# Performance work log

Measured on AMD Instinct MI355X. Metric: run time of the kernel, lower is better.

## Reference

```python
import jax, jax.numpy as jnp
import numpy as np
from jax import lax

B, T, E, H, N_LAYERS = 64, 256, 512, 512, 2


def _lstm_stack(x, params):
    # x: [B, T, in] -> returns full top-layer hidden sequence [T, B, H]
    xs = jnp.swapaxes(x, 0, 1)  # time-major [T, B, in]
    for (Wih, Whh, bih, bhh) in params:
        def step(carry, xt, Wih=Wih, Whh=Whh, bih=bih, bhh=bhh):
            h, c = carry
            gates = xt @ Wih.T + bih + h @ Whh.T + bhh  # [B, 4H]
            i, f, g, o = jnp.split(gates, 4, axis=-1)   # PyTorch gate order i,f,g,o
            i = jax.nn.sigmoid(i)
            f = jax.nn.sigmoid(f)
            g = jnp.tanh(g)
            o = jax.nn.sigmoid(o)
            c = f * c + i * g
            h = o * jnp.tanh(c)
            return (h, c), h
        nb = xs.shape[1]
        hdim = Whh.shape[1]
        init = (jnp.zeros((nb, hdim), xs.dtype), jnp.zeros((nb, hdim), xs.dtype))
        _, xs = lax.scan(step, init, xs)
    return xs  # [T, B, H]


def setup_inputs() -> dict:
    key = jax.random.key(0)
    ks = jax.random.split(key, 16)
    s = 0.04  # ~1/sqrt(H) init scale
    inp = {"text": jax.random.normal(ks[0], (B, T, E), dtype=jnp.float32)}
    # layer 0: input dim E; layer 1: input dim H
    inp["W_ih0"] = jax.random.normal(ks[1], (4 * H, E), dtype=jnp.float32) * s
    inp["W_hh0"] = jax.random.normal(ks[2], (4 * H, H), dtype=jnp.float32) * s
    inp["b_ih0"] = jax.random.normal(ks[3], (4 * H,), dtype=jnp.float32) * s
    inp["b_hh0"] = jax.random.normal(ks[4], (4 * H,), dtype=jnp.float32) * s
    inp["W_ih1"] = jax.random.normal(ks[5], (4 * H, H), dtype=jnp.float32) * s
    inp["W_hh1"] = jax.random.normal(ks[6], (4 * H, H), dtype=jnp.float32) * s
    inp["b_ih1"] = jax.random.normal(ks[7], (4 * H,), dtype=jnp.float32) * s
    inp["b_hh1"] = jax.random.normal(ks[8], (4 * H,), dtype=jnp.float32) * s
    inp["W_lin"] = jax.random.normal(ks[9], (1, 2 * H), dtype=jnp.float32) * s
    inp["b_lin"] = jax.random.normal(ks[10], (1,), dtype=jnp.float32) * s
    return inp


def reference(text, W_ih0, W_hh0, b_ih0, b_hh0, W_ih1, W_hh1, b_ih1, b_hh1, W_lin, b_lin):
    params = [(W_ih0, W_hh0, b_ih0, b_hh0), (W_ih1, W_hh1, b_ih1, b_hh1)]
    out_f = _lstm_stack(text, params)[-1]                       # [B, H] last step, fwd pass
    out_r = _lstm_stack(jnp.flip(text, axis=1), params)[-1]     # [B, H] last step, reversed input (same weights, as in source)
    out = jnp.concatenate([out_f, out_r], axis=1)               # [B, 2H]
    # dropout is identity in eval mode
    return out @ W_lin.T + b_lin                                # [B, 1]
```

## Files before the change

kernel.cpp:

```cpp
#include <hip/hip_runtime.h>
#include <stdint.h>

constexpr int HD   = 512;
constexpr int TS   = 256;
constexpr int NB   = 64;
constexpr int MBR  = 128;
constexpr int SLAB = MBR * HD;

typedef __attribute__((ext_vector_type(8))) short bf16x8;
typedef __attribute__((ext_vector_type(4))) float f32x4;

__device__ __forceinline__ unsigned short f2bf(float f){
  union { float f; unsigned u; } v; v.f = f;
  unsigned r = v.u + 0x7fffu + ((v.u >> 16) & 1u);
  return (unsigned short)(r >> 16);
}
__device__ __forceinline__ float fsig(float x){ return 1.f / (1.f + __expf(-x)); }
__device__ __forceinline__ float ftanh(float x){ return 1.f - 2.f / (__expf(2.f * x) + 1.f); }
__device__ __forceinline__ void vdrain(){ asm volatile("s_waitcnt vmcnt(0)" ::: "memory"); }

__device__ __forceinline__ int ld_flag_sc1(const int* p){
  int v;
  asm volatile("global_load_dword %0, %1, off sc0 sc1\n\ts_waitcnt vmcnt(0)"
               : "=v"(v) : "v"(p) : "memory");
  return v;
}
__device__ __forceinline__ void st_sc1_b32(void* p, int v){
  asm volatile("global_store_dword %0, %1, off sc0 sc1" :: "v"(p), "v"(v) : "memory");
}

#define LD16_DEF(NAME, TAIL)                                                    \
__device__ __forceinline__ void NAME(const void* p, f32x4* r){                  \
  asm volatile(                                                                 \
    "global_load_dwordx4 %0,  %16, off sc0 sc1\n\t"                             \
    "global_load_dwordx4 %1,  %16, off offset:64 sc0 sc1\n\t"                   \
    "global_load_dwordx4 %2,  %16, off offset:128 sc0 sc1\n\t"                  \
    "global_load_dwordx4 %3,  %16, off offset:192 sc0 sc1\n\t"                  \
    "global_load_dwordx4 %4,  %16, off offset:256 sc0 sc1\n\t"                  \
    "global_load_dwordx4 %5,  %16, off offset:320 sc0 sc1\n\t"                  \
    "global_load_dwordx4 %6,  %16, off offset:384 sc0 sc1\n\t"                  \
    "global_load_dwordx4 %7,  %16, off offset:448 sc0 sc1\n\t"                  \
    "global_load_dwordx4 %8,  %16, off offset:512 sc0 sc1\n\t"                  \
    "global_load_dwordx4 %9,  %16, off offset:576 sc0 sc1\n\t"                  \
    "global_load_dwordx4 %10, %16, off offset:640 sc0 sc1\n\t"                  \
    "global_load_dwordx4 %11, %16, off offset:704 sc0 sc1\n\t"                  \
    "global_load_dwordx4 %12, %16, off offset:768 sc0 sc1\n\t"                  \
    "global_load_dwordx4 %13, %16, off offset:832 sc0 sc1\n\t"                  \
    "global_load_dwordx4 %14, %16, off offset:896 sc0 sc1\n\t"                  \
    "global_load_dwordx4 %15, %16, off offset:960 sc0 sc1\n\t"                  \
    TAIL                                                                        \
    : "=&v"(r[0]), "=&v"(r[1]), "=&v"(r[2]), "=&v"(r[3]),                       \
      "=&v"(r[4]), "=&v"(r[5]), "=&v"(r[6]), "=&v"(r[7]),                       \
      "=&v"(r[8]), "=&v"(r[9]), "=&v"(r[10]), "=&v"(r[11]),                     \
      "=&v"(r[12]), "=&v"(r[13]), "=&v"(r[14]), "=&v"(r[15])                    \
    : "v"(p) : "memory");                                                       \
}
LD16_DEF(ld16_sc1,       "s_waitcnt vmcnt(0)")
LD16_DEF(ld16_sc1_issue, "s_nop 0")

__device__ __forceinline__ bf16x8 pack8(float4 a, float4 b){
  bf16x8 w;
  w[0]=(short)f2bf(a.x); w[1]=(short)f2bf(a.y); w[2]=(short)f2bf(a.z); w[3]=(short)f2bf(a.w);
  w[4]=(short)f2bf(b.x); w[5]=(short)f2bf(b.y); w[6]=(short)f2bf(b.z); w[7]=(short)f2bf(b.w);
  return w;
}

__global__ __launch_bounds__(512, 1)
void lstm_persist(const float* __restrict__ text,
                  const float* __restrict__ Wih0, const float* __restrict__ Whh0,
                  const float* __restrict__ bih0, const float* __restrict__ bhh0,
                  const float* __restrict__ Wih1, const float* __restrict__ Whh1,
                  const float* __restrict__ bih1, const float* __restrict__ bhh1,
                  unsigned short* __restrict__ h0x,
                  unsigned short* __restrict__ h1r,
                  float* __restrict__ H1f,
                  int* __restrict__ F)
{
  extern __shared__ unsigned short Blds[];
  __shared__ int s_abort;

  const int wg    = blockIdx.x;
  const int layer = wg >> 7;
  const int grp   = (wg >> 5) & 3;
  const int slice = wg & 31;
  const int m0    = grp * 32;
  const int u0    = slice * 16;
  const int tid   = threadIdx.x;
  const int wv    = tid >> 6;
  const int l     = tid & 63;
  const int lj    = l & 15;
  const int lk    = l >> 4;
  const int wgrp  = wv & 3;
  const int mi    = wv >> 2;

  if (tid == 0) s_abort = 0;

  int* F0g = F + (0 + grp) * (TS * 32);
  int* F1g = F + (4 + grp) * (TS * 32);

  const float* Wihl = layer ? Wih1 : Wih0;
  const float* Whhl = layer ? Whh1 : Whh0;
  for (int it = tid; it < 64 * 128; it += 512){
    int c = it >> 7, kg = it & 127;
    int unit = u0 + ((c >> 4) << 2) + ((c & 15) >> 2);
    int gate = c & 3;
    const float* s = (kg < 64) ? (Wihl + (size_t)(gate * HD + unit) * HD + kg * 8)
                               : (Whhl + (size_t)(gate * HD + unit) * HD + (kg - 64) * 8);
    *(bf16x8*)((char*)Blds + c * 2048 + ((kg ^ (c & 7)) << 4)) =
        pack8(((const float4*)s)[0], ((const float4*)s)[1]);
  }

  const int myunit = u0 + (wgrp << 2) + (lj >> 2);
  const int mygate = lj & 3;
  const float bgv  = (layer ? bih1 : bih0)[mygate * HD + myunit]
                   + (layer ? bhh1 : bhh0)[mygate * HD + myunit];
  const int aoff   = (m0 + mi * 16 + lj) * HD + lk * 8;
  const int cboff  = (wgrp * 16 + lj) * 2048;
  const int swz    = lj & 7;

  float cst[4] = {0.f, 0.f, 0.f, 0.f};
  __syncthreads();

  auto ldsB = [&](int kg)->bf16x8 {
    return *(const bf16x8*)((const char*)Blds + cboff + ((kg ^ swz) << 4));
  };
  auto pollwait = [&](const int* pA, const int* pB){
    if (*(volatile int*)&s_abort) return;
    const int* fp = (l < 32) ? (pA + l) : (pB + (l - 32));
    int it = 0;
    for (;;){
      int v = ld_flag_sc1(fp);
      if (__all(v != 0)) break;
      if (++it > 2000000){ s_abort = 1; break; }
      __builtin_amdgcn_s_sleep(1);
    }
  };
  auto cellstore = [&](const f32x4& aP, const f32x4& aQ,
                       unsigned short* __restrict__ hslab, bool wrF){
    #pragma unroll
    for (int r = 0; r < 4; ++r){
      float v  = aP[r] + aQ[r] + bgv;
      float v1 = __shfl_xor(v, 1);
      float v2 = __shfl_xor(v, 2);
      float v3 = __shfl_xor(v, 3);
      auto pick = [&](int m)->float {
        return m == 0 ? v : (m == 1 ? v1 : (m == 2 ? v2 : v3));
      };
      float gi = pick(mygate);
      float gf = pick(mygate ^ 1);
      float gg = pick(mygate ^ 2);
      float go = pick(mygate ^ 3);
      float i_ = fsig(gi);
      float f_ = fsig(gf);
      float g_ = ftanh(gg);
      float o_ = fsig(go);
      float c  = f_ * cst[r] + i_ * g_;
      cst[r] = c;
      float h  = o_ * ftanh(c);
      int row  = m0 + mi * 16 + lk * 4 + r;
      int hb   = (int)f2bf(h);
      int pb   = __shfl_xor(hb, 4);
      if ((lj & 7) == 0)
        st_sc1_b32((char*)hslab + ((size_t)row * HD + myunit) * 2,
                   (hb & 0xffff) | (pb << 16));
      if (wrF && mygate == 0)
        H1f[(size_t)row * HD + myunit] = h;
    }
  };
  auto preX = [&](int t, f32x4& acc){
    int ar  = m0 + mi * 16 + lj;
    int b   = ar & 63;
    int ts2 = (ar < 64) ? t : (TS - 1 - t);
    const float* src = text + ((size_t)b * TS + ts2) * HD + lk * 8;
    acc = (f32x4){0.f, 0.f, 0.f, 0.f};
    #pragma unroll
    for (int kk = 0; kk < 16; ++kk){
      const float* s = src + kk * 32;
      bf16x8 a = pack8(((const float4*)s)[0], ((const float4*)s)[1]);
      acc = __builtin_amdgcn_mfma_f32_16x16x32_bf16(a, ldsB(kk * 4 + lk), acc, 0, 0, 0);
    }
  };

  if (layer == 0){
    f32x4 accPre;
    preX(0, accPre);
    for (int t = 0; t < TS; ++t){
      if (t > 0){
        if (wv == 0) pollwait(F0g + (t - 1) * 32, F0g + (t - 1) * 32);
        __syncthreads();
      }
      f32x4 accPost = {0.f, 0.f, 0.f, 0.f};
      if (t > 0){
        f32x4 raw[16];
        ld16_sc1(h0x + (size_t)(t - 1) * SLAB + aoff, raw);
        #pragma unroll
        for (int kk = 0; kk < 16; ++kk)
          accPost = __builtin_amdgcn_mfma_f32_16x16x32_bf16(
                      __builtin_bit_cast(bf16x8, raw[kk]), ldsB(64 + kk * 4 + lk),
                      accPost, 0, 0, 0);
      }
      cellstore(accPre, accPost, h0x + (size_t)t * SLAB, false);
      vdrain();
      __syncthreads();
      if (tid == 0) st_sc1_b32(F0g + t * 32 + slice, 1);
      if (t + 1 < TS) preX(t + 1, accPre);
    }
  } else {
    for (int t = 0; t < TS; ++t){
      if (wv == 0){
        const int* pA = (t > 0) ? (F1g + (t - 1) * 32) : (F0g + 0);
        pollwait(pA, F0g + t * 32);
      }
      __syncthreads();
      f32x4 rawI[16], rawR[16];
      if (t > 0){
        ld16_sc1_issue(h0x + (size_t)t * SLAB + aoff, rawI);
        ld16_sc1(h1r + (size_t)((t - 1) & 3) * SLAB + aoff, rawR);
      } else {
        ld16_sc1(h0x + aoff, rawI);
      }
      f32x4 accPre  = {0.f, 0.f, 0.f, 0.f};
      f32x4 accPost = {0.f, 0.f, 0.f, 0.f};
      #pragma unroll
      for (int kk = 0; kk < 16; ++kk)
        accPre = __builtin_amdgcn_mfma_f32_16x16x32_bf16(
                   __builtin_bit_cast(bf16x8, rawI[kk]), ldsB(kk * 4 + lk),
                   accPre, 0, 0, 0);
      if (t > 0){
        #pragma unroll
        for (int kk = 0; kk < 16; ++kk)
          accPost = __builtin_amdgcn_mfma_f32_16x16x32_bf16(
                      __builtin_bit_cast(bf16x8, rawR[kk]), ldsB(64 + kk * 4 + lk),
                      accPost, 0, 0, 0);
      }
      cellstore(accPre, accPost, h1r + (size_t)(t & 3) * SLAB, t == TS - 1);
      vdrain();
      __syncthreads();
      if (tid == 0) st_sc1_b32(F1g + t * 32 + slice, 1);
    }
  }
}

__global__ void final_linear(const float* __restrict__ H1f, const float* __restrict__ Wlin,
                             const float* __restrict__ blin, float* __restrict__ out){
  int b = blockIdx.x, l = threadIdx.x;
  float s = 0.f;
  for (int j = l; j < HD; j += 64) s += H1f[(size_t)b * HD + j]        * Wlin[j];
  for (int j = l; j < HD; j += 64) s += H1f[(size_t)(NB + b) * HD + j] * Wlin[HD + j];
  #pragma unroll
  for (int off = 32; off; off >>= 1) s += __shfl_down(s, off);
  if (l == 0) out[b] = s + blin[0];
}

extern "C" void kernel_launch(void* const* d_in, const int* in_sizes, int n_in,
                              void* d_out, int out_size, void* d_ws, size_t ws_size,
                              hipStream_t stream)
{
  const float* text = (const float*)d_in[0];
  const float* Wih0 = (const float*)d_in[1];
  const float* Whh0 = (const float*)d_in[2];
  const float* bih0 = (const float*)d_in[3];
  const float* bhh0 = (const float*)d_in[4];
  const float* Wih1 = (const float*)d_in[5];
  const float* Whh1 = (const float*)d_in[6];
  const float* bih1 = (const float*)d_in[7];
  const float* bhh1 = (const float*)d_in[8];
  const float* Wlin = (const float*)d_in[9];
  const float* blin = (const float*)d_in[10];

  uint8_t* p = (uint8_t*)d_ws;
  unsigned short* h0x = (unsigned short*)p; p += (size_t)TS * SLAB * 2;
  unsigned short* h1r = (unsigned short*)p; p += (size_t)4 * SLAB * 2;
  float* H1f          = (float*)p;          p += (size_t)SLAB * 4;
  int* F              = (int*)p;            p += (size_t)8 * TS * 32 * 4;

  hipMemsetAsync(F, 0, (size_t)8 * TS * 32 * 4, stream);

  hipFuncSetAttribute((const void*)lstm_persist,
                      hipFuncAttributeMaxDynamicSharedMemorySize, 131072);

  const float* A0 = text;
  const float *A1 = Wih0, *A2 = Whh0, *A3 = bih0, *A4 = bhh0;
  const float *A5 = Wih1, *A6 = Whh1, *A7 = bih1, *A8 = bhh1;
  unsigned short* B0 = h0x; unsigned short* B1 = h1r;
  float* B2 = H1f; int* B3 = F;
  void* args[] = {(void*)&A0,
                  (void*)&A1, (void*)&A2, (void*)&A3, (void*)&A4,
                  (void*)&A5, (void*)&A6, (void*)&A7, (void*)&A8,
                  (void*)&B0, (void*)&B1, (void*)&B2, (void*)&B3};
  hipLaunchCooperativeKernel((void*)lstm_persist, dim3(256), dim3(512),
                             args, 131072, stream);

  final_linear<<<NB, 64, 0, stream>>>(H1f, Wlin, blin, (float*)d_out);
}
```

Before: 3.722 ms.

## Collapse batch-row groups into each workgroup, cutting grid from 256 to 64

```diff
diff --git a/kernel.cpp b/kernel.cpp
--- a/kernel.cpp
+++ b/kernel.cpp
@@ -29,35 +29,31 @@
   asm volatile("global_store_dword %0, %1, off sc0 sc1" :: "v"(p), "v"(v) : "memory");
 }
 
-#define LD16_DEF(NAME, TAIL)                                                    \
-__device__ __forceinline__ void NAME(const void* p, f32x4* r){                  \
-  asm volatile(                                                                 \
-    "global_load_dwordx4 %0,  %16, off sc0 sc1\n\t"                             \
-    "global_load_dwordx4 %1,  %16, off offset:64 sc0 sc1\n\t"                   \
-    "global_load_dwordx4 %2,  %16, off offset:128 sc0 sc1\n\t"                  \
-    "global_load_dwordx4 %3,  %16, off offset:192 sc0 sc1\n\t"                  \
-    "global_load_dwordx4 %4,  %16, off offset:256 sc0 sc1\n\t"                  \
-    "global_load_dwordx4 %5,  %16, off offset:320 sc0 sc1\n\t"                  \
-    "global_load_dwordx4 %6,  %16, off offset:384 sc0 sc1\n\t"                  \
-    "global_load_dwordx4 %7,  %16, off offset:448 sc0 sc1\n\t"                  \
-    "global_load_dwordx4 %8,  %16, off offset:512 sc0 sc1\n\t"                  \
-    "global_load_dwordx4 %9,  %16, off offset:576 sc0 sc1\n\t"                  \
-    "global_load_dwordx4 %10, %16, off offset:640 sc0 sc1\n\t"                  \
-    "global_load_dwordx4 %11, %16, off offset:704 sc0 sc1\n\t"                  \
-    "global_load_dwordx4 %12, %16, off offset:768 sc0 sc1\n\t"                  \
-    "global_load_dwordx4 %13, %16, off offset:832 sc0 sc1\n\t"                  \
-    "global_load_dwordx4 %14, %16, off offset:896 sc0 sc1\n\t"                  \
-    "global_load_dwordx4 %15, %16, off offset:960 sc0 sc1\n\t"                  \
-    TAIL                                                                        \
-    : "=&v"(r[0]), "=&v"(r[1]), "=&v"(r[2]), "=&v"(r[3]),                       \
-      "=&v"(r[4]), "=&v"(r[5]), "=&v"(r[6]), "=&v"(r[7]),                       \
-      "=&v"(r[8]), "=&v"(r[9]), "=&v"(r[10]), "=&v"(r[11]),                     \
-      "=&v"(r[12]), "=&v"(r[13]), "=&v"(r[14]), "=&v"(r[15])                    \
-    : "v"(p) : "memory");                                                       \
-}
-LD16_DEF(ld16_sc1,       "s_waitcnt vmcnt(0)")
-LD16_DEF(ld16_sc1_issue, "s_nop 0")
-
+__device__ __forceinline__ void ld16_sc1(const void* p, f32x4* r){
+  asm volatile(
+    "global_load_dwordx4 %0,  %16, off sc0 sc1\n\t"
+    "global_load_dwordx4 %1,  %16, off offset:64 sc0 sc1\n\t"
+    "global_load_dwordx4 %2,  %16, off offset:128 sc0 sc1\n\t"
+    "global_load_dwordx4 %3,  %16, off offset:192 sc0 sc1\n\t"
+    "global_load_dwordx4 %4,  %16, off offset:256 sc0 sc1\n\t"
+    "global_load_dwordx4 %5,  %16, off offset:320 sc0 sc1\n\t"
+    "global_load_dwordx4 %6,  %16, off offset:384 sc0 sc1\n\t"
+    "global_load_dwordx4 %7,  %16, off offset:448 sc0 sc1\n\t"
+    "global_load_dwordx4 %8,  %16, off offset:512 sc0 sc1\n\t"
+    "global_load_dwordx4 %9,  %16, off offset:576 sc0 sc1\n\t"
+    "global_load_dwordx4 %10, %16, off offset:640 sc0 sc1\n\t"
+    "global_load_dwordx4 %11, %16, off offset:704 sc0 sc1\n\t"
+    "global_load_dwordx4 %12, %16, off offset:768 sc0 sc1\n\t"
+    "global_load_dwordx4 %13, %16, off offset:832 sc0 sc1\n\t"
+    "global_load_dwordx4 %14, %16, off offset:896 sc0 sc1\n\t"
+    "global_load_dwordx4 %15, %16, off offset:960 sc0 sc1\n\t"
+    "s_waitcnt vmcnt(0)"
+    : "=&v"(r[0]), "=&v"(r[1]), "=&v"(r[2]), "=&v"(r[3]),
+      "=&v"(r[4]), "=&v"(r[5]), "=&v"(r[6]), "=&v"(r[7]),
+      "=&v"(r[8]), "=&v"(r[9]), "=&v"(r[10]), "=&v"(r[11]),
+      "=&v"(r[12]), "=&v"(r[13]), "=&v"(r[14]), "=&v"(r[15])
+    : "v"(p) : "memory");
+}
 __device__ __forceinline__ bf16x8 pack8(float4 a, float4 b){
   bf16x8 w;
   w[0]=(short)f2bf(a.x); w[1]=(short)f2bf(a.y); w[2]=(short)f2bf(a.z); w[3]=(short)f2bf(a.w);
@@ -80,23 +76,20 @@
   __shared__ int s_abort;
 
   const int wg    = blockIdx.x;
-  const int layer = wg >> 7;
-  const int grp   = (wg >> 5) & 3;
+  const int layer = wg >> 5;
   const int slice = wg & 31;
-  const int m0    = grp * 32;
   const int u0    = slice * 16;
   const int tid   = threadIdx.x;
   const int wv    = tid >> 6;
   const int l     = tid & 63;
   const int lj    = l & 15;
   const int lk    = l >> 4;
-  const int wgrp  = wv & 3;
-  const int mi    = wv >> 2;
+  const int mi    = wv;
 
   if (tid == 0) s_abort = 0;
 
-  int* F0g = F + (0 + grp) * (TS * 32);
-  int* F1g = F + (4 + grp) * (TS * 32);
+  int* F0 = F;
+  int* F1 = F + TS * 32;
 
   const float* Wihl = layer ? Wih1 : Wih0;
   const float* Whhl = layer ? Whh1 : Whh0;
@@ -110,23 +103,28 @@
         pack8(((const float4*)s)[0], ((const float4*)s)[1]);
   }
 
-  const int myunit = u0 + (wgrp << 2) + (lj >> 2);
   const int mygate = lj & 3;
-  const float bgv  = (layer ? bih1 : bih0)[mygate * HD + myunit]
-                   + (layer ? bhh1 : bhh0)[mygate * HD + myunit];
-  const int aoff   = (m0 + mi * 16 + lj) * HD + lk * 8;
-  const int cboff  = (wgrp * 16 + lj) * 2048;
-  const int swz    = lj & 7;
-
-  float cst[4] = {0.f, 0.f, 0.f, 0.f};
+  const int usub   = lj >> 2;
+  float bgv[4];
+  #pragma unroll
+  for (int cf = 0; cf < 4; ++cf){
+    int unit = u0 + cf * 4 + usub;
+    bgv[cf] = (layer ? bih1 : bih0)[mygate * HD + unit]
+            + (layer ? bhh1 : bhh0)[mygate * HD + unit];
+  }
+  const int arow = mi * 16 + lj;
+  const int aoff = arow * HD + lk * 8;
+  const int swz  = lj & 7;
+
+  float cst[4][4] = {};
   __syncthreads();
 
-  auto ldsB = [&](int kg)->bf16x8 {
-    return *(const bf16x8*)((const char*)Blds + cboff + ((kg ^ swz) << 4));
-  };
-  auto pollwait = [&](const int* pA, const int* pB){
+  auto ldsB = [&](int cf, int kg)->bf16x8 {
+    return *(const bf16x8*)((const char*)Blds + (cf * 16 + lj) * 2048 + ((kg ^ swz) << 4));
+  };
+  auto pollwait = [&](const int* base){
     if (*(volatile int*)&s_abort) return;
-    const int* fp = (l < 32) ? (pA + l) : (pB + (l - 32));
+    const int* fp = base + (l & 31);
     int it = 0;
     for (;;){
       int v = ld_flag_sc1(fp);
@@ -135,108 +133,122 @@
       __builtin_amdgcn_s_sleep(1);
     }
   };
-  auto cellstore = [&](const f32x4& aP, const f32x4& aQ,
+  auto mfmaHalf = [&](const f32x4* raw, int gb, f32x4* acc){
+    #pragma unroll
+    for (int kk = 0; kk < 16; ++kk){
+      bf16x8 a = __builtin_bit_cast(bf16x8, raw[kk]);
+      #pragma unroll
+      for (int cf = 0; cf < 4; ++cf)
+        acc[cf] = __builtin_amdgcn_mfma_f32_16x16x32_bf16(
+                    a, ldsB(cf, gb + kk * 4 + lk), acc[cf], 0, 0, 0);
+    }
+  };
+  auto cellstore = [&](const f32x4* aP, const f32x4* aQ,
                        unsigned short* __restrict__ hslab, bool wrF){
     #pragma unroll
-    for (int r = 0; r < 4; ++r){
-      float v  = aP[r] + aQ[r] + bgv;
-      float v1 = __shfl_xor(v, 1);
-      float v2 = __shfl_xor(v, 2);
-      float v3 = __shfl_xor(v, 3);
-      auto pick = [&](int m)->float {
-        return m == 0 ? v : (m == 1 ? v1 : (m == 2 ? v2 : v3));
-      };
-      float gi = pick(mygate);
-      float gf = pick(mygate ^ 1);
-      float gg = pick(mygate ^ 2);
-      float go = pick(mygate ^ 3);
-      float i_ = fsig(gi);
-      float f_ = fsig(gf);
-      float g_ = ftanh(gg);
-      float o_ = fsig(go);
-      float c  = f_ * cst[r] + i_ * g_;
-      cst[r] = c;
-      float h  = o_ * ftanh(c);
-      int row  = m0 + mi * 16 + lk * 4 + r;
-      int hb   = (int)f2bf(h);
-      int pb   = __shfl_xor(hb, 4);
-      if ((lj & 7) == 0)
-        st_sc1_b32((char*)hslab + ((size_t)row * HD + myunit) * 2,
-                   (hb & 0xffff) | (pb << 16));
-      if (wrF && mygate == 0)
-        H1f[(size_t)row * HD + myunit] = h;
-    }
-  };
-  auto preX = [&](int t, f32x4& acc){
-    int ar  = m0 + mi * 16 + lj;
-    int b   = ar & 63;
-    int ts2 = (ar < 64) ? t : (TS - 1 - t);
+    for (int cf = 0; cf < 4; ++cf){
+      #pragma unroll
+      for (int r = 0; r < 4; ++r){
+        float v  = aP[cf][r] + aQ[cf][r] + bgv[cf];
+        float v1 = __shfl_xor(v, 1);
+        float v2 = __shfl_xor(v, 2);
+        float v3 = __shfl_xor(v, 3);
+        auto pick = [&](int m)->float {
+          return m == 0 ? v : (m == 1 ? v1 : (m == 2 ? v2 : v3));
+        };
+        float gi = pick(mygate);
+        float gf = pick(mygate ^ 1);
+        float gg = pick(mygate ^ 2);
+        float go = pick(mygate ^ 3);
+        float i_ = fsig(gi);
+        float f_ = fsig(gf);
+        float g_ = ftanh(gg);
+        float o_ = fsig(go);
+        float c  = f_ * cst[cf][r] + i_ * g_;
+        cst[cf][r] = c;
+        float h  = o_ * ftanh(c);
+        int row  = mi * 16 + lk * 4 + r;
+        int unit = u0 + cf * 4 + usub;
+        int hb   = (int)f2bf(h);
+        int pb   = __shfl_xor(hb, 4);
+        if ((lj & 7) == 0)
+          st_sc1_b32((char*)hslab + ((size_t)row * HD + unit) * 2,
+                     (hb & 0xffff) | (pb << 16));
+        if (wrF && mygate == 0)
+          H1f[(size_t)row * HD + unit] = h;
+      }
+    }
+  };
+  auto preX = [&](int t, f32x4* acc){
+    int b   = arow & 63;
+    int ts2 = (arow < 64) ? t : (TS - 1 - t);
     const float* src = text + ((size_t)b * TS + ts2) * HD + lk * 8;
-    acc = (f32x4){0.f, 0.f, 0.f, 0.f};
+    #pragma unroll
+    for (int cf = 0; cf < 4; ++cf) acc[cf] = (f32x4){0.f, 0.f, 0.f, 0.f};
     #pragma unroll
     for (int kk = 0; kk < 16; ++kk){
       const float* s = src + kk * 32;
       bf16x8 a = pack8(((const float4*)s)[0], ((const float4*)s)[1]);
-      acc = __builtin_amdgcn_mfma_f32_16x16x32_bf16(a, ldsB(kk * 4 + lk), acc, 0, 0, 0);
-    }
-  };
+      #pragma unroll
+      for (int cf = 0; cf < 4; ++cf)
+        acc[cf] = __builtin_amdgcn_mfma_f32_16x16x32_bf16(
+                    a, ldsB(cf, kk * 4 + lk), acc[cf], 0, 0, 0);
+    }
+  };
+
+  f32x4 accPre[4], accPost[4];
 
   if (layer == 0){
-    f32x4 accPre;
     preX(0, accPre);
     for (int t = 0; t < TS; ++t){
+      #pragma unroll
+      for (int cf = 0; cf < 4; ++cf) accPost[cf] = (f32x4){0.f, 0.f, 0.f, 0.f};
       if (t > 0){
-        if (wv == 0) pollwait(F0g + (t - 1) * 32, F0g + (t - 1) * 32);
+        if (wv == 0) pollwait(F0 + (t - 1) * 32);
         __syncthreads();
-      }
-      f32x4 accPost = {0.f, 0.f, 0.f, 0.f};
-      if (t > 0){
         f32x4 raw[16];
         ld16_sc1(h0x + (size_t)(t - 1) * SLAB + aoff, raw);
-        #pragma unroll
-        for (int kk = 0; kk < 16; ++kk)
-          accPost = __builtin_amdgcn_mfma_f32_16x16x32_bf16(
-                      __builtin_bit_cast(bf16x8, raw[kk]), ldsB(64 + kk * 4 + lk),
-                      accPost, 0, 0, 0);
+        mfmaHalf(raw, 64, accPost);
       }
       cellstore(accPre, accPost, h0x + (size_t)t * SLAB, false);
       vdrain();
       __syncthreads();
-      if (tid == 0) st_sc1_b32(F0g + t * 32 + slice, 1);
+      if (tid == 0) st_sc1_b32(F0 + t * 32 + slice, 1);
       if (t + 1 < TS) preX(t + 1, accPre);
     }
   } else {
+    if (wv == 0) pollwait(F0 + 0);
+    __syncthreads();
+    {
+      f32x4 raw[16];
+      ld16_sc1(h0x + aoff, raw);
+      #pragma unroll
+      for (int cf = 0; cf < 4; ++cf) accPre[cf] = (f32x4){0.f, 0.f, 0.f, 0.f};
+      mfmaHalf(raw, 0, accPre);
+    }
     for (int t = 0; t < TS; ++t){
-      if (wv == 0){
-        const int* pA = (t > 0) ? (F1g + (t - 1) * 32) : (F0g + 0);
-        pollwait(pA, F0g + t * 32);
-      }
-      __syncthreads();
-      f32x4 rawI[16], rawR[16];
+      #pragma unroll
+      for (int cf = 0; cf < 4; ++cf) accPost[cf] = (f32x4){0.f, 0.f, 0.f, 0.f};
       if (t > 0){
-        ld16_sc1_issue(h0x + (size_t)t * SLAB + aoff, rawI);
-        ld16_sc1(h1r + (size_t)((t - 1) & 3) * SLAB + aoff, rawR);
-      } else {
-        ld16_sc1(h0x + aoff, rawI);
-      }
-      f32x4 accPre  = {0.f, 0.f, 0.f, 0.f};
-      f32x4 accPost = {0.f, 0.f, 0.f, 0.f};
-      #pragma unroll
-      for (int kk = 0; kk < 16; ++kk)
-        accPre = __builtin_amdgcn_mfma_f32_16x16x32_bf16(
-                   __builtin_bit_cast(bf16x8, rawI[kk]), ldsB(kk * 4 + lk),
-                   accPre, 0, 0, 0);
-      if (t > 0){
-        #pragma unroll
-        for (int kk = 0; kk < 16; ++kk)
-          accPost = __builtin_amdgcn_mfma_f32_16x16x32_bf16(
-                      __builtin_bit_cast(bf16x8, rawR[kk]), ldsB(64 + kk * 4 + lk),
-                      accPost, 0, 0, 0);
+        if (wv == 0) pollwait(F1 + (t - 1) * 32);
+        __syncthreads();
+        f32x4 raw[16];
+        ld16_sc1(h1r + (size_t)((t - 1) & 3) * SLAB + aoff, raw);
+        mfmaHalf(raw, 64, accPost);
       }
       cellstore(accPre, accPost, h1r + (size_t)(t & 3) * SLAB, t == TS - 1);
       vdrain();
       __syncthreads();
-      if (tid == 0) st_sc1_b32(F1g + t * 32 + slice, 1);
+      if (tid == 0) st_sc1_b32(F1 + t * 32 + slice, 1);
+      if (t + 1 < TS){
+        if (wv == 0) pollwait(F0 + (t + 1) * 32);
+        __syncthreads();
+        f32x4 raw[16];
+        ld16_sc1(h0x + (size_t)(t + 1) * SLAB + aoff, raw);
+        #pragma unroll
+        for (int cf = 0; cf < 4; ++cf) accPre[cf] = (f32x4){0.f, 0.f, 0.f, 0.f};
+        mfmaHalf(raw, 0, accPre);
+      }
     }
   }
 }
@@ -272,9 +284,9 @@
   unsigned short* h0x = (unsigned short*)p; p += (size_t)TS * SLAB * 2;
   unsigned short* h1r = (unsigned short*)p; p += (size_t)4 * SLAB * 2;
   float* H1f          = (float*)p;          p += (size_t)SLAB * 4;
-  int* F              = (int*)p;            p += (size_t)8 * TS * 32 * 4;
-
-  hipMemsetAsync(F, 0, (size_t)8 * TS * 32 * 4, stream);
+  int* F              = (int*)p;            p += (size_t)2 * TS * 32 * 4;
+
+  hipMemsetAsync(F, 0, (size_t)2 * TS * 32 * 4, stream);
 
   hipFuncSetAttribute((const void*)lstm_persist,
                       hipFuncAttributeMaxDynamicSharedMemorySize, 131072);
@@ -288,7 +300,7 @@
                   (void*)&A1, (void*)&A2, (void*)&A3, (void*)&A4,
                   (void*)&A5, (void*)&A6, (void*)&A7, (void*)&A8,
                   (void*)&B0, (void*)&B1, (void*)&B2, (void*)&B3};
-  hipLaunchCooperativeKernel((void*)lstm_persist, dim3(256), dim3(512),
+  hipLaunchCooperativeKernel((void*)lstm_persist, dim3(64), dim3(512),
                              args, 131072, stream);
 
   final_linear<<<NB, 64, 0, stream>>>(H1f, Wlin, blin, (float*)d_out);
```

Measured after the change: 10.07 ms. 171% more time.

## Repartition LSTM workgroups to 16-row groups and keep recurrent weights in registers

Applied to the files above, without the earlier changes.

```diff
diff --git a/kernel.cpp b/kernel.cpp
--- a/kernel.cpp
+++ b/kernel.cpp
@@ -6,6 +6,8 @@
 constexpr int NB   = 64;
 constexpr int MBR  = 128;
 constexpr int SLAB = MBR * HD;
+constexpr int NG   = 8;
+constexpr int NS   = 16;
 
 typedef __attribute__((ext_vector_type(8))) short bf16x8;
 typedef __attribute__((ext_vector_type(4))) float f32x4;
@@ -29,35 +31,31 @@
   asm volatile("global_store_dword %0, %1, off sc0 sc1" :: "v"(p), "v"(v) : "memory");
 }
 
-#define LD16_DEF(NAME, TAIL)                                                    \
-__device__ __forceinline__ void NAME(const void* p, f32x4* r){                  \
-  asm volatile(                                                                 \
-    "global_load_dwordx4 %0,  %16, off sc0 sc1\n\t"                             \
-    "global_load_dwordx4 %1,  %16, off offset:64 sc0 sc1\n\t"                   \
-    "global_load_dwordx4 %2,  %16, off offset:128 sc0 sc1\n\t"                  \
-    "global_load_dwordx4 %3,  %16, off offset:192 sc0 sc1\n\t"                  \
-    "global_load_dwordx4 %4,  %16, off offset:256 sc0 sc1\n\t"                  \
-    "global_load_dwordx4 %5,  %16, off offset:320 sc0 sc1\n\t"                  \
-    "global_load_dwordx4 %6,  %16, off offset:384 sc0 sc1\n\t"                  \
-    "global_load_dwordx4 %7,  %16, off offset:448 sc0 sc1\n\t"                  \
-    "global_load_dwordx4 %8,  %16, off offset:512 sc0 sc1\n\t"                  \
-    "global_load_dwordx4 %9,  %16, off offset:576 sc0 sc1\n\t"                  \
-    "global_load_dwordx4 %10, %16, off offset:640 sc0 sc1\n\t"                  \
-    "global_load_dwordx4 %11, %16, off offset:704 sc0 sc1\n\t"                  \
-    "global_load_dwordx4 %12, %16, off offset:768 sc0 sc1\n\t"                  \
-    "global_load_dwordx4 %13, %16, off offset:832 sc0 sc1\n\t"                  \
-    "global_load_dwordx4 %14, %16, off offset:896 sc0 sc1\n\t"                  \
-    "global_load_dwordx4 %15, %16, off offset:960 sc0 sc1\n\t"                  \
-    TAIL                                                                        \
-    : "=&v"(r[0]), "=&v"(r[1]), "=&v"(r[2]), "=&v"(r[3]),                       \
-      "=&v"(r[4]), "=&v"(r[5]), "=&v"(r[6]), "=&v"(r[7]),                       \
-      "=&v"(r[8]), "=&v"(r[9]), "=&v"(r[10]), "=&v"(r[11]),                     \
-      "=&v"(r[12]), "=&v"(r[13]), "=&v"(r[14]), "=&v"(r[15])                    \
-    : "v"(p) : "memory");                                                       \
-}
-LD16_DEF(ld16_sc1,       "s_waitcnt vmcnt(0)")
-LD16_DEF(ld16_sc1_issue, "s_nop 0")
-
+__device__ __forceinline__ void ld16_sc1(const void* p, f32x4* r){
+  asm volatile(
+    "global_load_dwordx4 %0,  %16, off sc0 sc1\n\t"
+    "global_load_dwordx4 %1,  %16, off offset:64 sc0 sc1\n\t"
+    "global_load_dwordx4 %2,  %16, off offset:128 sc0 sc1\n\t"
+    "global_load_dwordx4 %3,  %16, off offset:192 sc0 sc1\n\t"
+    "global_load_dwordx4 %4,  %16, off offset:256 sc0 sc1\n\t"
+    "global_load_dwordx4 %5,  %16, off offset:320 sc0 sc1\n\t"
+    "global_load_dwordx4 %6,  %16, off offset:384 sc0 sc1\n\t"
+    "global_load_dwordx4 %7,  %16, off offset:448 sc0 sc1\n\t"
+    "global_load_dwordx4 %8,  %16, off offset:512 sc0 sc1\n\t"
+    "global_load_dwordx4 %9,  %16, off offset:576 sc0 sc1\n\t"
+    "global_load_dwordx4 %10, %16, off offset:640 sc0 sc1\n\t"
+    "global_load_dwordx4 %11, %16, off offset:704 sc0 sc1\n\t"
+    "global_load_dwordx4 %12, %16, off offset:768 sc0 sc1\n\t"
+    "global_load_dwordx4 %13, %16, off offset:832 sc0 sc1\n\t"
+    "global_load_dwordx4 %14, %16, off offset:896 sc0 sc1\n\t"
+    "global_load_dwordx4 %15, %16, off offset:960 sc0 sc1\n\t"
+    "s_waitcnt vmcnt(0)"
+    : "=&v"(r[0]), "=&v"(r[1]), "=&v"(r[2]), "=&v"(r[3]),
+      "=&v"(r[4]), "=&v"(r[5]), "=&v"(r[6]), "=&v"(r[7]),
+      "=&v"(r[8]), "=&v"(r[9]), "=&v"(r[10]), "=&v"(r[11]),
+      "=&v"(r[12]), "=&v"(r[13]), "=&v"(r[14]), "=&v"(r[15])
+    : "v"(p) : "memory");
+}
 __device__ __forceinline__ bf16x8 pack8(float4 a, float4 b){
   bf16x8 w;
   w[0]=(short)f2bf(a.x); w[1]=(short)f2bf(a.y); w[2]=(short)f2bf(a.z); w[3]=(short)f2bf(a.w);
@@ -81,42 +79,50 @@
 
   const int wg    = blockIdx.x;
   const int layer = wg >> 7;
-  const int grp   = (wg >> 5) & 3;
-  const int slice = wg & 31;
-  const int m0    = grp * 32;
-  const int u0    = slice * 16;
+  const int grp   = (wg >> 4) & 7;
+  const int slice = wg & 15;
+  const int m0    = grp * 16;
+  const int u0    = slice * 32;
   const int tid   = threadIdx.x;
   const int wv    = tid >> 6;
   const int l     = tid & 63;
   const int lj    = l & 15;
   const int lk    = l >> 4;
-  const int wgrp  = wv & 3;
-  const int mi    = wv >> 2;
 
   if (tid == 0) s_abort = 0;
 
-  int* F0g = F + (0 + grp) * (TS * 32);
-  int* F1g = F + (4 + grp) * (TS * 32);
+  int* F0g = F + ((0 * NG + grp) * TS) * NS;
+  int* F1g = F + ((1 * NG + grp) * TS) * NS;
 
   const float* Wihl = layer ? Wih1 : Wih0;
   const float* Whhl = layer ? Whh1 : Whh0;
-  for (int it = tid; it < 64 * 128; it += 512){
-    int c = it >> 7, kg = it & 127;
-    int unit = u0 + ((c >> 4) << 2) + ((c & 15) >> 2);
+
+  for (int it = tid; it < 128 * 64; it += 512){
+    int c = it >> 6, kg = it & 63;
+    int unit = u0 + (c >> 2);
     int gate = c & 3;
-    const float* s = (kg < 64) ? (Wihl + (size_t)(gate * HD + unit) * HD + kg * 8)
-                               : (Whhl + (size_t)(gate * HD + unit) * HD + (kg - 64) * 8);
-    *(bf16x8*)((char*)Blds + c * 2048 + ((kg ^ (c & 7)) << 4)) =
+    const float* s = Wihl + (size_t)(gate * HD + unit) * HD + kg * 8;
+    *(bf16x8*)((char*)Blds + c * 1024 + ((kg ^ (c & 7)) << 4)) =
         pack8(((const float4*)s)[0], ((const float4*)s)[1]);
   }
 
-  const int myunit = u0 + (wgrp << 2) + (lj >> 2);
-  const int mygate = lj & 3;
-  const float bgv  = (layer ? bih1 : bih0)[mygate * HD + myunit]
-                   + (layer ? bhh1 : bhh0)[mygate * HD + myunit];
-  const int aoff   = (m0 + mi * 16 + lj) * HD + lk * 8;
-  const int cboff  = (wgrp * 16 + lj) * 2048;
-  const int swz    = lj & 7;
+  const int j      = wv * 16 + lj;
+  const int myunit = u0 + (j >> 2);
+  const int mygate = j & 3;
+  bf16x8 bPost[16];
+  {
+    const float* s0 = Whhl + (size_t)(mygate * HD + myunit) * HD + lk * 8;
+    #pragma unroll
+    for (int kk = 0; kk < 16; ++kk){
+      const float* s = s0 + kk * 32;
+      bPost[kk] = pack8(((const float4*)s)[0], ((const float4*)s)[1]);
+    }
+  }
+  const float bgv = (layer ? bih1 : bih0)[mygate * HD + myunit]
+                  + (layer ? bhh1 : bhh0)[mygate * HD + myunit];
+  const int aoff  = (m0 + lj) * HD + lk * 8;
+  const int cboff = j * 1024;
+  const int swz   = lj & 7;
 
   float cst[4] = {0.f, 0.f, 0.f, 0.f};
   __syncthreads();
@@ -124,9 +130,9 @@
   auto ldsB = [&](int kg)->bf16x8 {
     return *(const bf16x8*)((const char*)Blds + cboff + ((kg ^ swz) << 4));
   };
-  auto pollwait = [&](const int* pA, const int* pB){
+  auto pollwait = [&](const int* base){
     if (*(volatile int*)&s_abort) return;
-    const int* fp = (l < 32) ? (pA + l) : (pB + (l - 32));
+    const int* fp = base + (l & 15);
     int it = 0;
     for (;;){
       int v = ld_flag_sc1(fp);
@@ -134,6 +140,12 @@
       if (++it > 2000000){ s_abort = 1; break; }
       __builtin_amdgcn_s_sleep(1);
     }
+  };
+  auto postHalf = [&](const f32x4* raw, f32x4& acc){
+    #pragma unroll
+    for (int kk = 0; kk < 16; ++kk)
+      acc = __builtin_amdgcn_mfma_f32_16x16x32_bf16(
+              __builtin_bit_cast(bf16x8, raw[kk]), bPost[kk], acc, 0, 0, 0);
   };
   auto cellstore = [&](const f32x4& aP, const f32x4& aQ,
                        unsigned short* __restrict__ hslab, bool wrF){
@@ -157,10 +169,10 @@
       float c  = f_ * cst[r] + i_ * g_;
       cst[r] = c;
       float h  = o_ * ftanh(c);
-      int row  = m0 + mi * 16 + lk * 4 + r;
+      int row  = m0 + lk * 4 + r;
       int hb   = (int)f2bf(h);
       int pb   = __shfl_xor(hb, 4);
-      if ((lj & 7) == 0)
+      if ((j & 7) == 0)
         st_sc1_b32((char*)hslab + ((size_t)row * HD + myunit) * 2,
                    (hb & 0xffff) | (pb << 16));
       if (wrF && mygate == 0)
@@ -168,9 +180,9 @@
     }
   };
   auto preX = [&](int t, f32x4& acc){
-    int ar  = m0 + mi * 16 + lj;
-    int b   = ar & 63;
-    int ts2 = (ar < 64) ? t : (TS - 1 - t);
+    int arow = m0 + lj;
+    int b    = arow & 63;
+    int ts2  = (arow < 64) ? t : (TS - 1 - t);
     const float* src = text + ((size_t)b * TS + ts2) * HD + lk * 8;
     acc = (f32x4){0.f, 0.f, 0.f, 0.f};
     #pragma unroll
@@ -185,58 +197,46 @@
     f32x4 accPre;
     preX(0, accPre);
     for (int t = 0; t < TS; ++t){
-      if (t > 0){
-        if (wv == 0) pollwait(F0g + (t - 1) * 32, F0g + (t - 1) * 32);
-        __syncthreads();
-      }
       f32x4 accPost = {0.f, 0.f, 0.f, 0.f};
       if (t > 0){
+        if (wv == 0) pollwait(F0g + (t - 1) * NS);
+        __syncthreads();
         f32x4 raw[16];
         ld16_sc1(h0x + (size_t)(t - 1) * SLAB + aoff, raw);
-        #pragma unroll
-        for (int kk = 0; kk < 16; ++kk)
-          accPost = __builtin_amdgcn_mfma_f32_16x16x32_bf16(
-                      __builtin_bit_cast(bf16x8, raw[kk]), ldsB(64 + kk * 4 + lk),
-                      accPost, 0, 0, 0);
+        postHalf(raw, accPost);
       }
       cellstore(accPre, accPost, h0x + (size_t)t * SLAB, false);
       vdrain();
       __syncthreads();
-      if (tid == 0) st_sc1_b32(F0g + t * 32 + slice, 1);
+      if (tid == 0) st_sc1_b32(F0g + t * NS + slice, 1);
       if (t + 1 < TS) preX(t + 1, accPre);
     }
   } else {
     for (int t = 0; t < TS; ++t){
-      if (wv == 0){
-        const int* pA = (t > 0) ? (F1g + (t - 1) * 32) : (F0g + 0);
-        pollwait(pA, F0g + t * 32);
-      }
+      if (wv == 0) pollwait(F0g + t * NS);
       __syncthreads();
-      f32x4 rawI[16], rawR[16];
-      if (t > 0){
-        ld16_sc1_issue(h0x + (size_t)t * SLAB + aoff, rawI);
-        ld16_sc1(h1r + (size_t)((t - 1) & 3) * SLAB + aoff, rawR);
-      } else {
-        ld16_sc1(h0x + aoff, rawI);
-      }
-      f32x4 accPre  = {0.f, 0.f, 0.f, 0.f};
-      f32x4 accPost = {0.f, 0.f, 0.f, 0.f};
-      #pragma unroll
-      for (int kk = 0; kk < 16; ++kk)
-        accPre = __builtin_amdgcn_mfma_f32_16x16x32_bf16(
-                   __builtin_bit_cast(bf16x8, rawI[kk]), ldsB(kk * 4 + lk),
-                   accPre, 0, 0, 0);
-      if (t > 0){
+      f32x4 accPre = {0.f, 0.f, 0.f, 0.f};
+      {
+        f32x4 rawI[16];
+        ld16_sc1(h0x + (size_t)t * SLAB + aoff, rawI);
         #pragma unroll
         for (int kk = 0; kk < 16; ++kk)
-          accPost = __builtin_amdgcn_mfma_f32_16x16x32_bf16(
-                      __builtin_bit_cast(bf16x8, rawR[kk]), ldsB(64 + kk * 4 + lk),
-                      accPost, 0, 0, 0);
+          accPre = __builtin_amdgcn_mfma_f32_16x16x32_bf16(
+                     __builtin_bit_cast(bf16x8, rawI[kk]), ldsB(kk * 4 + lk),
+                     accPre, 0, 0, 0);
+      }
+      f32x4 accPost = {0.f, 0.f, 0.f, 0.f};
+      if (t > 0){
+        if (wv == 0) pollwait(F1g + (t - 1) * NS);
+        __syncthreads();
+        f32x4 rawR[16];
+        ld16_sc1(h1r + (size_t)((t - 1) & 3) * SLAB + aoff, rawR);
+        postHalf(rawR, accPost);
       }
       cellstore(accPre, accPost, h1r + (size_t)(t & 3) * SLAB, t == TS - 1);
       vdrain();
       __syncthreads();
-      if (tid == 0) st_sc1_b32(F1g + t * 32 + slice, 1);
+      if (tid == 0) st_sc1_b32(F1g + t * NS + slice, 1);
     }
   }
 }
@@ -245,8 +245,8 @@
                              const float* __restrict__ blin, float* __restrict__ out){
   int b = blockIdx.x, l = threadIdx.x;
   float s = 0.f;
-  for (int j = l; j < HD; j += 64) s += H1f[(size_t)b * HD + j]        * Wlin[j];
-  for (int j = l; j < HD; j += 64) s += H1f[(size_t)(NB + b) * HD + j] * Wlin[HD + j];
+  for (int jj = l; jj < HD; jj += 64) s += H1f[(size_t)b * HD + jj]        * Wlin[jj];
+  for (int jj = l; jj < HD; jj += 64) s += H1f[(size_t)(NB + b) * HD + jj] * Wlin[HD + jj];
   #pragma unroll
   for (int off = 32; off; off >>= 1) s += __shfl_down(s, off);
   if (l == 0) out[b] = s + blin[0];
@@ -272,9 +272,9 @@
   unsigned short* h0x = (unsigned short*)p; p += (size_t)TS * SLAB * 2;
   unsigned short* h1r = (unsigned short*)p; p += (size_t)4 * SLAB * 2;
   float* H1f          = (float*)p;          p += (size_t)SLAB * 4;
-  int* F              = (int*)p;            p += (size_t)8 * TS * 32 * 4;
-
-  hipMemsetAsync(F, 0, (size_t)8 * TS * 32 * 4, stream);
+  int* F              = (int*)p;            p += (size_t)2 * NG * TS * NS * 4;
+
+  hipMemsetAsync(F, 0, (size_t)2 * NG * TS * NS * 4, stream);
 
   hipFuncSetAttribute((const void*)lstm_persist,
                       hipFuncAttributeMaxDynamicSharedMemorySize, 131072);
```

Result: faster. 3.497 ms (-6.0%).
